# Kernel optimization log

Hardware: AMD Instinct MI355X
Metric: run time of the kernel (lower is better)

Reference implementation:

```python
import jax, jax.numpy as jnp
import numpy as np

M = 0.5
S = 64.0
LS_EPS = 0.0
COS_M = float(np.cos(M))
SIN_M = float(np.sin(M))
THRESHOLD = float(np.cos(np.pi - M))
MM = float(np.sin(np.pi - M) * M)
N_CLASSES = 100000


def setup_inputs() -> dict:
    key = jax.random.key(0)
    k1, k2, k3 = jax.random.split(key, 3)
    embeddings = jax.random.normal(k1, (1024, 512), dtype=jnp.float32)
    kernel = jax.random.normal(k2, (512, N_CLASSES), dtype=jnp.float32) * 0.01
    t = jnp.zeros((1,), dtype=jnp.float32)
    label = jax.random.randint(k3, (1024,), 0, N_CLASSES, dtype=jnp.int64)
    return {"embeddings": embeddings, "kernel": kernel, "t": t, "label": label}


def reference(embeddings, kernel, t, label):
    # l2-normalize embeddings over feature axis, kernel over input axis
    emb = embeddings / jnp.linalg.norm(embeddings, axis=1, keepdims=True)
    kn = kernel / jnp.linalg.norm(kernel, axis=0, keepdims=True)
    cos_theta = jnp.clip(emb @ kn, -1.0, 1.0)  # [N, C]
    n = embeddings.shape[0]
    rows = jnp.arange(n)
    target_logit = cos_theta[rows, label][:, None]  # [N, 1]
    sin_theta = jnp.sqrt(1.0 - target_logit ** 2)
    cos_theta_m = target_logit * COS_M - sin_theta * SIN_M  # [N, 1]
    mask = cos_theta > cos_theta_m  # hard examples (broadcast per row)
    final_target_logit = jnp.where(target_logit > THRESHOLD,
                                   cos_theta_m, target_logit - MM)
    # running-mean buffer update (no-grad in original)
    t_new = jax.lax.stop_gradient(target_logit.mean() * 0.01 + 0.99 * t[0])
    cos_theta = jnp.where(mask, cos_theta * (t_new + cos_theta), cos_theta)
    cos_theta = cos_theta.at[rows, label].set(final_target_logit[:, 0])
    if LS_EPS > 0:
        cos_theta = (1 - LS_EPS) * cos_theta + LS_EPS / N_CLASSES
    return cos_theta * S
```

## Files before the change

### kernel.cpp

```cpp
#include <hip/hip_runtime.h>

typedef unsigned short u16;
typedef unsigned int u32;
typedef __attribute__((ext_vector_type(8))) short bf16x8;
typedef __attribute__((ext_vector_type(4))) float f32x4;

#define KDIM   512
#define NROWS  1024
#define NCLS   100000
#define CPAD   100096
#define NSTRIP 782
#define NMT    8

#define COS_M_C   0.8775825618903728f
#define SIN_M_C   0.4794255386042030f
#define THRESH_C  (-0.8775825618903728f)
#define MM_C      0.2397127693021015f
#define S_C       64.0f

__device__ __forceinline__ u16 f2bf(float f) {
    u32 x = __float_as_uint(f);
    x += 0x7fffu + ((x >> 16) & 1u);
    return (u16)(x >> 16);
}
__device__ __forceinline__ float bf2f(u16 u) {
    return __uint_as_float(((u32)u) << 16);
}

__device__ __forceinline__ void gld16(const void* g, void* l) {
    __builtin_amdgcn_global_load_lds(
        (const __attribute__((address_space(1))) void*)g,
        (__attribute__((address_space(3))) void*)l, 16, 0, 0);
}

__global__ __launch_bounds__(64)
void norm_emb_k(const float* __restrict__ emb, float* __restrict__ Af,
                u16* __restrict__ Aw) {
    const int i = blockIdx.x, l = threadIdx.x;
    const float* e = emb + i * KDIM;
    float4 v0 = *(const float4*)(e + l * 4);
    float4 v1 = *(const float4*)(e + 256 + l * 4);
    float s = v0.x*v0.x + v0.y*v0.y + v0.z*v0.z + v0.w*v0.w
            + v1.x*v1.x + v1.y*v1.y + v1.z*v1.z + v1.w*v1.w;
    #pragma unroll
    for (int o = 1; o < 64; o <<= 1) s += __shfl_xor(s, o);
    float inv = rsqrtf(s);
    float4 n0 = make_float4(v0.x*inv, v0.y*inv, v0.z*inv, v0.w*inv);
    float4 n1 = make_float4(v1.x*inv, v1.y*inv, v1.z*inv, v1.w*inv);
    *(float4*)(Af + i*KDIM + l*4)       = n0;
    *(float4*)(Af + i*KDIM + 256 + l*4) = n1;
    ushort4 p0 = { f2bf(n0.x), f2bf(n0.y), f2bf(n0.z), f2bf(n0.w) };
    ushort4 p1 = { f2bf(n1.x), f2bf(n1.y), f2bf(n1.z), f2bf(n1.w) };
    *(ushort4*)(Aw + i*KDIM + l*4)       = p0;
    *(ushort4*)(Aw + i*KDIM + 256 + l*4) = p1;
}

__global__ __launch_bounds__(128)
void transpose_norm_k(const float* __restrict__ Kg, u16* __restrict__ Bn,
                      float* __restrict__ kinv) {
    __shared__ float Ls[32 * 132];
    const int t  = threadIdx.x;
    const int jb = blockIdx.x * 128;
    const int j  = jb + t;
    u16* bstrip = Bn + (size_t)blockIdx.x * 65536;
    float acc = 0.f;
    for (int kc = 0; kc < 16; ++kc) {
        #pragma unroll
        for (int it = 0; it < 8; ++it) {
            int fid  = it * 128 + t;
            int r    = fid >> 5;
            int c4   = (fid & 31) * 4;
            int gcol = jb + c4;
            float4 v;
            if (gcol + 3 < NCLS) {
                v = *(const float4*)(Kg + (kc*32 + r) * NCLS + gcol);
            } else {
                v.x = (gcol + 0 < NCLS) ? Kg[(kc*32 + r)*NCLS + gcol + 0] : 0.f;
                v.y = (gcol + 1 < NCLS) ? Kg[(kc*32 + r)*NCLS + gcol + 1] : 0.f;
                v.z = (gcol + 2 < NCLS) ? Kg[(kc*32 + r)*NCLS + gcol + 2] : 0.f;
                v.w = (gcol + 3 < NCLS) ? Kg[(kc*32 + r)*NCLS + gcol + 3] : 0.f;
            }
            *(float4*)(Ls + r * 132 + c4) = v;
        }
        __syncthreads();
        #pragma unroll
        for (int g = 0; g < 4; ++g) {
            u16 u[8];
            #pragma unroll
            for (int e = 0; e < 8; ++e) {
                float v = Ls[(g*8 + e) * 132 + t];
                acc += v * v;
                u[e] = f2bf(v);
            }
            uint4 w;
            w.x = (u32)u[0] | ((u32)u[1] << 16);
            w.y = (u32)u[2] | ((u32)u[3] << 16);
            w.z = (u32)u[4] | ((u32)u[5] << 16);
            w.w = (u32)u[6] | ((u32)u[7] << 16);
            *(uint4*)(bstrip + kc*4096 + t*32 + g*8) = w;
        }
        __syncthreads();
    }
    kinv[j] = rsqrtf(fmaxf(acc, 1e-30f));
}

__global__ __launch_bounds__(64)
void target_k(const float* __restrict__ Af, const u16* __restrict__ Bn,
              const float* __restrict__ kinv, const int* __restrict__ label,
              float* __restrict__ tgt, float* __restrict__ ctm,
              float* __restrict__ fin) {
    const int i = blockIdx.x, l = threadIdx.x;
    const int lab = label[i];
    const float* a = Af + i * KDIM + l * 8;
    float4 a0 = *(const float4*)a;
    float4 a1 = *(const float4*)(a + 4);
    uint4 bv = *(const uint4*)(Bn + (size_t)(lab >> 7) * 65536
                               + (l >> 2) * 4096 + (lab & 127) * 32 + (l & 3) * 8);
    float d = a0.x * bf2f((u16)(bv.x & 0xffff)) + a0.y * bf2f((u16)(bv.x >> 16))
            + a0.z * bf2f((u16)(bv.y & 0xffff)) + a0.w * bf2f((u16)(bv.y >> 16))
            + a1.x * bf2f((u16)(bv.z & 0xffff)) + a1.y * bf2f((u16)(bv.z >> 16))
            + a1.z * bf2f((u16)(bv.w & 0xffff)) + a1.w * bf2f((u16)(bv.w >> 16));
    #pragma unroll
    for (int o = 1; o < 64; o <<= 1) d += __shfl_xor(d, o);
    if (l == 0) {
        float c = d * kinv[lab];
        c = fminf(fmaxf(c, -1.f), 1.f);
        tgt[i] = c;
        float sn = sqrtf(fmaxf(1.f - c*c, 0.f));
        float cm = c * COS_M_C - sn * SIN_M_C;
        ctm[i] = cm;
        fin[i] = (c > THRESH_C) ? cm : (c - MM_C);
    }
}

__global__ __launch_bounds__(256)
void tnew_k(const float* __restrict__ tgt, const float* __restrict__ tin,
            float* __restrict__ tnw) {
    __shared__ float red[256];
    const int t = threadIdx.x;
    float s = tgt[t] + tgt[t + 256] + tgt[t + 512] + tgt[t + 768];
    red[t] = s;
    __syncthreads();
    for (int o = 128; o > 0; o >>= 1) {
        if (t < o) red[t] += red[t + o];
        __syncthreads();
    }
    if (t == 0) tnw[0] = red[0] * (0.01f / 1024.f) + 0.99f * tin[0];
}

__global__ __launch_bounds__(256)
void gemm_k(const u16* __restrict__ A, const u16* __restrict__ B,
            const float* __restrict__ kinv, const float* __restrict__ ctm,
            const float* __restrict__ fin, const int* __restrict__ label,
            const float* __restrict__ tnwp, float* __restrict__ out) {
    __shared__ __align__(16) u16 As[2][4096];
    __shared__ __align__(16) u16 Bs[2][4096];
    const int tid  = threadIdx.x;
    const int wave = tid >> 6, lane = tid & 63;

    const int L  = blockIdx.x;
    const int w  = (L & 7) * NSTRIP + (L >> 3);
    const int mt = w & 7;
    const int cs = w >> 3;
    const int m0 = mt * 128;
    const int j0 = cs * 128;
    const int wr = (wave >> 1) * 64;
    const int wc = (wave & 1) * 64;

    f32x4 acc[4][4] = {};

    const int o0 = tid * 16;
    const int o1 = o0 + 4096;
    const int rA0 = o0 >> 6, cA0 = (o0 & 63) >> 1;
    const int rA1 = o1 >> 6, cA1 = (o1 & 63) >> 1;
    const u16* gA0 = A + (m0 + rA0) * KDIM + cA0;
    const u16* gA1 = A + (m0 + rA1) * KDIM + cA1;
    const u16* gB0 = B + (size_t)cs * 65536 + (o0 >> 1);
    const u16* gB1 = gB0 + 2048;
    const int lOff0 = o0 >> 1;
    const int lOff1 = lOff0 + 2048;

    const int aOff = (wr + (lane & 15)) * 64 + (lane >> 4) * 16;
    const int bOff = (wc + (lane & 15)) * 64 + (lane >> 4) * 16;

#define STAGE(b, ks)                                            \
    do {                                                        \
        gld16(gA0 + (ks) * 32, &As[b][lOff0]);                  \
        gld16(gA1 + (ks) * 32, &As[b][lOff1]);                  \
        gld16(gB0 + (ks) * 4096, &Bs[b][lOff0]);                \
        gld16(gB1 + (ks) * 4096, &Bs[b][lOff1]);                \
    } while (0)

    STAGE(0, 0);
    int cur = 0;
    #pragma unroll 2
    for (int ks = 0; ks < 16; ++ks) {
        if (ks < 15) {
            STAGE(cur ^ 1, ks + 1);
            asm volatile("s_waitcnt vmcnt(4)" ::: "memory");
        } else {
            asm volatile("s_waitcnt vmcnt(0)" ::: "memory");
        }
        __builtin_amdgcn_s_barrier();
        __builtin_amdgcn_sched_barrier(0);

        const char* aB = (const char*)As[cur] + aOff;
        const char* bB = (const char*)Bs[cur] + bOff;
        bf16x8 af[4], bfr[4];
        #pragma unroll
        for (int m = 0; m < 4; ++m)
            af[m] = *(const bf16x8*)(aB + m * 1024);
        #pragma unroll
        for (int n = 0; n < 4; ++n)
            bfr[n] = *(const bf16x8*)(bB + n * 1024);
        #pragma unroll
        for (int m = 0; m < 4; ++m)
            #pragma unroll
            for (int n = 0; n < 4; ++n)
                acc[m][n] = __builtin_amdgcn_mfma_f32_16x16x32_bf16(
                                af[m], bfr[n], acc[m][n], 0, 0, 0);

        asm volatile("s_waitcnt lgkmcnt(0)" ::: "memory");
        __builtin_amdgcn_s_barrier();
        __builtin_amdgcn_sched_barrier(0);
        cur ^= 1;
    }
#undef STAGE

    const float tnew = *tnwp;
    const int colbase = j0 + wc + (lane & 15);
    float kv[4];
    int cols[4];
    #pragma unroll
    for (int n = 0; n < 4; ++n) {
        cols[n] = colbase + n * 16;
        kv[n] = (cols[n] < NCLS) ? kinv[cols[n]] : 0.f;
    }
    #pragma unroll
    for (int m = 0; m < 4; ++m) {
        const int rb = m0 + wr + m * 16 + (lane >> 4) * 4;
        #pragma unroll
        for (int r = 0; r < 4; ++r) {
            const int row = rb + r;
            const int lab = label[row];
            const float ct = ctm[row];
            const float fv = fin[row];
            float* orow = out + (size_t)row * NCLS;
            #pragma unroll
            for (int n = 0; n < 4; ++n) {
                float c = acc[m][n][r] * kv[n];
                c = fminf(fmaxf(c, -1.f), 1.f);
                float v = (c > ct) ? c * (tnew + c) : c;
                v = (cols[n] == lab) ? fv : v;
                if (cols[n] < NCLS)
                    orow[cols[n]] = v * S_C;
            }
        }
    }
}

extern "C" void kernel_launch(void* const* d_in, const int* in_sizes, int n_in,
                              void* d_out, int out_size, void* d_ws, size_t ws_size,
                              hipStream_t stream) {
    const float* emb = (const float*)d_in[0];
    const float* Kg  = (const float*)d_in[1];
    const float* tin = (const float*)d_in[2];
    const int*   lab = (const int*)d_in[3];
    float* out = (float*)d_out;

    char* w = (char*)d_ws;
    u16*   Bn   = (u16*)w;
    u16*   Aw   = (u16*)(w + 102498304);
    float* Af   = (float*)(w + 103546880);
    float* kinv = (float*)(w + 105644032);
    float* tgt  = (float*)(w + 106044416);
    float* ctmv = (float*)(w + 106048512);
    float* finv = (float*)(w + 106052608);
    float* tnw  = (float*)(w + 106056704);

    norm_emb_k<<<NROWS, 64, 0, stream>>>(emb, Af, Aw);
    transpose_norm_k<<<NSTRIP, 128, 0, stream>>>(Kg, Bn, kinv);
    target_k<<<NROWS, 64, 0, stream>>>(Af, Bn, kinv, lab, tgt, ctmv, finv);
    tnew_k<<<1, 256, 0, stream>>>(tgt, tin, tnw);
    gemm_k<<<NSTRIP * NMT, 256, 0, stream>>>(
        Aw, Bn, kinv, ctmv, finv, lab, tnw, out);
}
```

Measured before the change: 415.3 us.

## Pre-swizzle A and B operands to avoid LDS bank conflicts and deepen prefetch

Result: faster. 370.0 us (-10.9%).

```diff
diff --git a/kernel.cpp b/kernel.cpp
--- a/kernel.cpp
+++ b/kernel.cpp
@@ -26,6 +26,12 @@
 __device__ __forceinline__ float bf2f(u16 u) {
     return __uint_as_float(((u32)u) << 16);
 }
+__device__ __forceinline__ u32 pack2(float a, float b) {
+    return (u32)f2bf(a) | ((u32)f2bf(b) << 16);
+}
+__device__ __forceinline__ int phi(int r, int q) {
+    return r * 4 + ((q + r + (r >> 1)) & 3);
+}
 
 __device__ __forceinline__ void gld16(const void* g, void* l) {
     __builtin_amdgcn_global_load_lds(
@@ -38,8 +44,8 @@
                 u16* __restrict__ Aw) {
     const int i = blockIdx.x, l = threadIdx.x;
     const float* e = emb + i * KDIM;
-    float4 v0 = *(const float4*)(e + l * 4);
-    float4 v1 = *(const float4*)(e + 256 + l * 4);
+    float4 v0 = *(const float4*)(e + l * 8);
+    float4 v1 = *(const float4*)(e + l * 8 + 4);
     float s = v0.x*v0.x + v0.y*v0.y + v0.z*v0.z + v0.w*v0.w
             + v1.x*v1.x + v1.y*v1.y + v1.z*v1.z + v1.w*v1.w;
     #pragma unroll
@@ -47,12 +53,16 @@
     float inv = rsqrtf(s);
     float4 n0 = make_float4(v0.x*inv, v0.y*inv, v0.z*inv, v0.w*inv);
     float4 n1 = make_float4(v1.x*inv, v1.y*inv, v1.z*inv, v1.w*inv);
-    *(float4*)(Af + i*KDIM + l*4)       = n0;
-    *(float4*)(Af + i*KDIM + 256 + l*4) = n1;
-    ushort4 p0 = { f2bf(n0.x), f2bf(n0.y), f2bf(n0.z), f2bf(n0.w) };
-    ushort4 p1 = { f2bf(n1.x), f2bf(n1.y), f2bf(n1.z), f2bf(n1.w) };
-    *(ushort4*)(Aw + i*KDIM + l*4)       = p0;
-    *(ushort4*)(Aw + i*KDIM + 256 + l*4) = p1;
+    *(float4*)(Af + i*KDIM + l*8)     = n0;
+    *(float4*)(Af + i*KDIM + l*8 + 4) = n1;
+    const int mt = i >> 7, g = (i >> 4) & 7, r = i & 15;
+    const int kc = l >> 2, q = l & 3;
+    uint4 w;
+    w.x = pack2(n0.x, n0.y);
+    w.y = pack2(n0.z, n0.w);
+    w.z = pack2(n1.x, n1.y);
+    w.w = pack2(n1.z, n1.w);
+    *(uint4*)(Aw + mt*65536 + kc*4096 + g*512 + phi(r, q)*8) = w;
 }
 
 __global__ __launch_bounds__(128)
@@ -84,11 +94,11 @@
         }
         __syncthreads();
         #pragma unroll
-        for (int g = 0; g < 4; ++g) {
+        for (int q = 0; q < 4; ++q) {
             u16 u[8];
             #pragma unroll
             for (int e = 0; e < 8; ++e) {
-                float v = Ls[(g*8 + e) * 132 + t];
+                float v = Ls[(q*8 + e) * 132 + t];
                 acc += v * v;
                 u[e] = f2bf(v);
             }
@@ -97,7 +107,7 @@
             w.y = (u32)u[2] | ((u32)u[3] << 16);
             w.z = (u32)u[4] | ((u32)u[5] << 16);
             w.w = (u32)u[6] | ((u32)u[7] << 16);
-            *(uint4*)(bstrip + kc*4096 + t*32 + g*8) = w;
+            *(uint4*)(bstrip + kc*4096 + (t>>4)*512 + phi(t & 15, q)*8) = w;
         }
         __syncthreads();
     }
@@ -115,7 +125,7 @@
     float4 a0 = *(const float4*)a;
     float4 a1 = *(const float4*)(a + 4);
     uint4 bv = *(const uint4*)(Bn + (size_t)(lab >> 7) * 65536
-                               + (l >> 2) * 4096 + (lab & 127) * 32 + (l & 3) * 8);
+               + (l >> 2) * 4096 + ((lab >> 4) & 7) * 512 + phi(lab & 15, l & 3) * 8);
     float d = a0.x * bf2f((u16)(bv.x & 0xffff)) + a0.y * bf2f((u16)(bv.x >> 16))
             + a0.z * bf2f((u16)(bv.y & 0xffff)) + a0.w * bf2f((u16)(bv.y >> 16))
             + a1.x * bf2f((u16)(bv.z & 0xffff)) + a1.y * bf2f((u16)(bv.z >> 16))
@@ -148,7 +158,7 @@
     if (t == 0) tnw[0] = red[0] * (0.01f / 1024.f) + 0.99f * tin[0];
 }
 
-__global__ __launch_bounds__(256)
+__global__ __launch_bounds__(256, 4)
 void gemm_k(const u16* __restrict__ A, const u16* __restrict__ B,
             const float* __restrict__ kinv, const float* __restrict__ ctm,
             const float* __restrict__ fin, const int* __restrict__ label,
@@ -169,61 +179,56 @@
 
     f32x4 acc[4][4] = {};
 
-    const int o0 = tid * 16;
-    const int o1 = o0 + 4096;
-    const int rA0 = o0 >> 6, cA0 = (o0 & 63) >> 1;
-    const int rA1 = o1 >> 6, cA1 = (o1 & 63) >> 1;
-    const u16* gA0 = A + (m0 + rA0) * KDIM + cA0;
-    const u16* gA1 = A + (m0 + rA1) * KDIM + cA1;
-    const u16* gB0 = B + (size_t)cs * 65536 + (o0 >> 1);
-    const u16* gB1 = gB0 + 2048;
-    const int lOff0 = o0 >> 1;
-    const int lOff1 = lOff0 + 2048;
-
-    const int aOff = (wr + (lane & 15)) * 64 + (lane >> 4) * 16;
-    const int bOff = (wc + (lane & 15)) * 64 + (lane >> 4) * 16;
-
-#define STAGE(b, ks)                                            \
-    do {                                                        \
-        gld16(gA0 + (ks) * 32, &As[b][lOff0]);                  \
-        gld16(gA1 + (ks) * 32, &As[b][lOff1]);                  \
-        gld16(gB0 + (ks) * 4096, &Bs[b][lOff0]);                \
-        gld16(gB1 + (ks) * 4096, &Bs[b][lOff1]);                \
-    } while (0)
+    const u16* gA = A + mt * 65536 + tid * 8;
+    const u16* gB = B + (size_t)cs * 65536 + tid * 8;
+    const int l0 = tid * 8, l1 = tid * 8 + 2048;
+
+    const int pphi = phi(lane & 15, lane >> 4) * 16;
+    const int aG = (wr >> 4) * 1024 + pphi;
+    const int bG = (wc >> 4) * 1024 + pphi;
+
+#define STAGE(b, ks) do {                               \
+    gld16(gA + (ks) * 4096,        &As[b][l0]);         \
+    gld16(gA + (ks) * 4096 + 2048, &As[b][l1]);         \
+    gld16(gB + (ks) * 4096,        &Bs[b][l0]);         \
+    gld16(gB + (ks) * 4096 + 2048, &Bs[b][l1]);         \
+} while (0)
 
     STAGE(0, 0);
-    int cur = 0;
-    #pragma unroll 2
+    STAGE(1, 1);
+    #pragma unroll
     for (int ks = 0; ks < 16; ++ks) {
-        if (ks < 15) {
-            STAGE(cur ^ 1, ks + 1);
-            asm volatile("s_waitcnt vmcnt(4)" ::: "memory");
-        } else {
-            asm volatile("s_waitcnt vmcnt(0)" ::: "memory");
-        }
+        const int cur = ks & 1;
+        if (ks < 15) asm volatile("s_waitcnt vmcnt(4)" ::: "memory");
+        else         asm volatile("s_waitcnt vmcnt(0)" ::: "memory");
         __builtin_amdgcn_s_barrier();
         __builtin_amdgcn_sched_barrier(0);
 
-        const char* aB = (const char*)As[cur] + aOff;
-        const char* bB = (const char*)Bs[cur] + bOff;
+        const char* ab = (const char*)As[cur] + aG;
+        const char* bb = (const char*)Bs[cur] + bG;
         bf16x8 af[4], bfr[4];
         #pragma unroll
         for (int m = 0; m < 4; ++m)
-            af[m] = *(const bf16x8*)(aB + m * 1024);
+            af[m] = *(const bf16x8*)(ab + m * 1024);
         #pragma unroll
         for (int n = 0; n < 4; ++n)
-            bfr[n] = *(const bf16x8*)(bB + n * 1024);
+            bfr[n] = *(const bf16x8*)(bb + n * 1024);
+
+        asm volatile("s_waitcnt lgkmcnt(0)" ::: "memory");
+        __builtin_amdgcn_sched_barrier(0);
+        __builtin_amdgcn_s_barrier();
+        __builtin_amdgcn_sched_barrier(0);
+
+        if (ks < 14) STAGE(cur, ks + 2);
+
+        __builtin_amdgcn_s_setprio(1);
         #pragma unroll
         for (int m = 0; m < 4; ++m)
             #pragma unroll
             for (int n = 0; n < 4; ++n)
                 acc[m][n] = __builtin_amdgcn_mfma_f32_16x16x32_bf16(
                                 af[m], bfr[n], acc[m][n], 0, 0, 0);
-
-        asm volatile("s_waitcnt lgkmcnt(0)" ::: "memory");
-        __builtin_amdgcn_s_barrier();
-        __builtin_amdgcn_sched_barrier(0);
-        cur ^= 1;
+        __builtin_amdgcn_s_setprio(0);
     }
 #undef STAGE
 
```
